# Kernel tuning notes

Measured on AMD Instinct MI355X. Metric: run time of the kernel, lower is better.

Reference implementation:

```python
import jax, jax.numpy as jnp
import numpy as np

N_NODES = 50000
N_REL = 4
N_EDGE = 160000
H = 128
OUT = 100
L_HID = 2
N_QUERY = 8192


def setup_inputs() -> dict:
    key = jax.random.key(0)
    ks = jax.random.split(key, 10)
    s = 1.0 / np.sqrt(H)
    return {
        "feature": jax.random.normal(ks[0], (N_NODES, H), dtype=jnp.float32),
        "Wr_h": jax.random.normal(ks[1], (L_HID, N_REL, H, H), dtype=jnp.float32) * s,
        "Ws_h": jax.random.normal(ks[2], (L_HID, H, H), dtype=jnp.float32) * s,
        "Wr_o": jax.random.normal(ks[3], (N_REL, H, OUT), dtype=jnp.float32) * s,
        "Ws_o": jax.random.normal(ks[4], (H, OUT), dtype=jnp.float32) * s,
        "edge_src": jax.random.randint(ks[5], (N_REL, N_EDGE), 0, N_NODES, dtype=jnp.int64),
        "edge_dst": jax.random.randint(ks[6], (N_REL, N_EDGE), 0, N_NODES, dtype=jnp.int64),
        "head_idx": jax.random.randint(ks[7], (N_QUERY,), 0, N_NODES, dtype=jnp.int64),
        "tail_idx": jax.random.randint(ks[8], (N_QUERY,), 0, N_NODES, dtype=jnp.int64),
    }


def _rgcn_layer(h, edge_src, edge_dst, inv_deg, Wr, Ws, activate):
    # per-relation gather of source features: [R, E, H]
    msgs = h[edge_src]
    # per-relation scatter-add into destination nodes: [R, N, H]
    agg = jax.vmap(lambda m, d: jax.ops.segment_sum(m, d, num_segments=h.shape[0]))(msgs, edge_dst)
    agg = agg * inv_deg[..., None]  # mean (right) normalization per relation
    out = h @ Ws + jnp.einsum("rnh,rho->no", agg, Wr)
    return jax.nn.relu(out) if activate else out


def reference(feature, Wr_h, Ws_h, Wr_o, Ws_o, edge_src, edge_dst, head_idx, tail_idx):
    n = feature.shape[0]
    # per-relation in-degree, computed once (graph structure is fixed)
    deg = jax.vmap(lambda d: jax.ops.segment_sum(
        jnp.ones(d.shape, feature.dtype), d, num_segments=n))(edge_dst)  # [R, N]
    inv_deg = 1.0 / jnp.maximum(deg, 1.0)
    h = feature
    for l in range(Wr_h.shape[0]):
        h = _rgcn_layer(h, edge_src, edge_dst, inv_deg, Wr_h[l], Ws_h[l], activate=True)
    h = _rgcn_layer(h, edge_src, edge_dst, inv_deg, Wr_o, Ws_o, activate=False)
    heads = h[head_idx]  # [Q, OUT]
    tails = h[tail_idx]  # [Q, OUT]
    return (heads, tails)
```

## Files before the change

### kernel.cpp

```cpp
#include <hip/hip_runtime.h>
#include <hip/hip_bf16.h>

#define NN 50000
#define NR 4
#define NE 160000
#define HD 128
#define OD 100
#define NQ 8192
#define NB_SCAN 196

#define NB_COUNT 2500
#define NB_CONV  6250
#define NB_PREPW 960

typedef __attribute__((ext_vector_type(8))) short bf16x8;
typedef __attribute__((ext_vector_type(4))) float f32x4;
typedef __attribute__((ext_vector_type(2))) float f32x2;
typedef __attribute__((ext_vector_type(4))) int int4v;

static __device__ __forceinline__ unsigned short f2bf(float f) {
    union { float f; unsigned int u; } v; v.f = f;
    unsigned int u = v.u;
    unsigned int r = u + 0x7FFFu + ((u >> 16) & 1u);
    return (unsigned short)(r >> 16);
}
static __device__ __forceinline__ float bflo(unsigned int v) {
    union { unsigned int u; float f; } x; x.u = v << 16; return x.f;
}
static __device__ __forceinline__ float bfhi(unsigned int v) {
    union { unsigned int u; float f; } x; x.u = v & 0xffff0000u; return x.f;
}


__global__ __launch_bounds__(256) void prep_merged_kernel(
        const int* __restrict__ edge_dst, int* __restrict__ deg,
        const float* __restrict__ feature, unsigned short* __restrict__ h,
        const float* __restrict__ Ws_h, const float* __restrict__ Wr_h,
        const float* __restrict__ Ws_o, const float* __restrict__ Wr_o,
        unsigned short* __restrict__ Wt) {
    const int b = blockIdx.x;
    if (b < NB_COUNT) {
        const int i = b * 256 + threadIdx.x;
        const int r = i / NE;
        atomicAdd(&deg[r * NN + edge_dst[i]], 1);
    } else if (b < NB_COUNT + NB_CONV) {
        const int i = ((b - NB_COUNT) * 256 + threadIdx.x) * 4;
        h[i + 0] = f2bf(feature[i + 0]);
        h[i + 1] = f2bf(feature[i + 1]);
        h[i + 2] = f2bf(feature[i + 2]);
        h[i + 3] = f2bf(feature[i + 3]);
    } else {
        const int idx = (b - NB_COUNT - NB_CONV) * 256 + threadIdx.x;
        const int l = idx / (128 * 640);
        const int rem = idx % (128 * 640);
        const int c = rem / 640;
        const int k = rem % 640;
        float v = 0.0f;
        if (l < 2) {
            if (k < HD) v = Ws_h[(l * HD + k) * HD + c];
            else {
                int r = (k - HD) >> 7, kk = (k - HD) & 127;
                v = Wr_h[((l * NR + r) * HD + kk) * HD + c];
            }
        } else if (c < OD) {
            if (k < HD) v = Ws_o[k * OD + c];
            else {
                int r = (k - HD) >> 7, kk = (k - HD) & 127;
                v = Wr_o[(r * HD + kk) * OD + c];
            }
        }
        Wt[idx] = f2bf(v);
    }
}


__global__ __launch_bounds__(256) void scanA_kernel(const int* __restrict__ deg,
                                                    int* __restrict__ excl,
                                                    int* __restrict__ bsum) {
    const int r = blockIdx.x / NB_SCAN;
    const int b = blockIdx.x % NB_SCAN;
    const int tid = threadIdx.x;
    const int idx = b * 256 + tid;
    int v = (idx < NN) ? deg[r * NN + idx] : 0;
    __shared__ int buf[256];
    buf[tid] = v; __syncthreads();
    int sum = v;
    for (int off = 1; off < 256; off <<= 1) {
        int t = (tid >= off) ? buf[tid - off] : 0;
        __syncthreads();
        sum += t; buf[tid] = sum;
        __syncthreads();
    }
    if (idx < NN) excl[r * NN + idx] = sum - v;
    if (tid == 255) bsum[r * NB_SCAN + b] = sum;
}

__global__ __launch_bounds__(256) void scanC_kernel(const int* __restrict__ excl,
                                                    const int* __restrict__ bsum,
                                                    int* __restrict__ row_start,
                                                    int* __restrict__ cursor) {
    const int r = blockIdx.x / NB_SCAN;
    const int b = blockIdx.x % NB_SCAN;
    const int tid = threadIdx.x;
    __shared__ int buf[256];
    buf[tid] = (tid < b) ? bsum[r * NB_SCAN + tid] : 0;
    __syncthreads();
    for (int off = 128; off > 0; off >>= 1) {
        if (tid < off) buf[tid] += buf[tid + off];
        __syncthreads();
    }
    const int prefix = buf[0];
    const int idx = b * 256 + tid;
    if (idx < NN) {
        int v = excl[r * NN + idx] + prefix;
        row_start[r * (NN + 1) + idx] = v;
        cursor[r * NN + idx] = v;
    }
    if (b == 0 && tid == 0) row_start[r * (NN + 1) + NN] = NE;
}

__global__ __launch_bounds__(256) void fill_csr_kernel(const int* __restrict__ edge_src,
                                                       const int* __restrict__ edge_dst,
                                                       int* __restrict__ cursor,
                                                       int* __restrict__ csr_src) {
    const int i = blockIdx.x * 256 + threadIdx.x;
    const int r = i / NE;
    const int dst = edge_dst[i];
    const int pos = atomicAdd(&cursor[r * NN + dst], 1);
    csr_src[r * NE + pos] = edge_src[i];
}


template<int MODE>
__global__ __launch_bounds__(512, 8)
void fused_kernel(const unsigned short* __restrict__ h,
                  const unsigned short* __restrict__ Bt,
                  const int* __restrict__ row_start,
                  const int* __restrict__ csr_src,
                  void* __restrict__ outp, int M) {
    __shared__ __align__(16) char lds[40960];
    const int tid = threadIdx.x;
    const int m0 = blockIdx.x * 32;
    const int lane = tid & 63;
    const int w = tid >> 6;

    {
        const int row = tid >> 4, kb = (tid & 15) * 16;
        int gr = m0 + row; if (gr >= M) gr = M - 1;
        int4v v = *(const int4v*)((const char*)h + (size_t)gr * 256 + kb);
        *(int4v*)(lds + row * 256 + (kb ^ ((row & 7) << 4))) = v;
    }

    {
        const int g = lane >> 4, li = lane & 15;
        const int* __restrict__ csr = csr_src + (size_t)g * NE;
        const char* hp = (const char*)h + li * 16;
        const int n0 = m0 + (w << 2);
        const int rsB = g * (NN + 1);

        int bnd[5];
#pragma unroll
        for (int i = 0; i < 5; i++) {
            int n = n0 + i; if (n > M) n = M;
            bnd[i] = row_start[rsB + n];
        }

#pragma unroll 1
        for (int i = 0; i < 4; ++i) {
            const int s = bnd[i], e = bnd[i + 1];

            int sj[8];
#pragma unroll
            for (int j = 0; j < 8; j++) sj[j] = (s + j < e) ? csr[s + j] : 0;

            int4v vj[8];
#pragma unroll
            for (int j = 0; j < 8; j++) {
                if (s + j < e) vj[j] = *(const int4v*)(hp + (size_t)sj[j] * 256);
                else           vj[j] = (int4v){0, 0, 0, 0};
            }
            __builtin_amdgcn_sched_barrier(0);

            f32x2 c0 = {0.f, 0.f}, c1 = {0.f, 0.f}, c2 = {0.f, 0.f}, c3 = {0.f, 0.f};
#pragma unroll
            for (int j = 0; j < 8; j++) {
                const unsigned int* vu = (const unsigned int*)&vj[j];
                c0 += (f32x2){bflo(vu[0]), bfhi(vu[0])};
                c1 += (f32x2){bflo(vu[1]), bfhi(vu[1])};
                c2 += (f32x2){bflo(vu[2]), bfhi(vu[2])};
                c3 += (f32x2){bflo(vu[3]), bfhi(vu[3])};
            }

            for (int t = s + 8; t < e; ++t) {
                const int src = csr[t];
                const int4v v = *(const int4v*)(hp + (size_t)src * 256);
                const unsigned int* vu = (const unsigned int*)&v;
                c0 += (f32x2){bflo(vu[0]), bfhi(vu[0])};
                c1 += (f32x2){bflo(vu[1]), bfhi(vu[1])};
                c2 += (f32x2){bflo(vu[2]), bfhi(vu[2])};
                c3 += (f32x2){bflo(vu[3]), bfhi(vu[3])};
            }

            const float inv = 1.0f / fmaxf((float)(e - s), 1.0f);
            unsigned int p0 = (unsigned int)f2bf(inv * c0[0]) | ((unsigned int)f2bf(inv * c0[1]) << 16);
            unsigned int p1 = (unsigned int)f2bf(inv * c1[0]) | ((unsigned int)f2bf(inv * c1[1]) << 16);
            unsigned int p2 = (unsigned int)f2bf(inv * c2[0]) | ((unsigned int)f2bf(inv * c2[1]) << 16);
            unsigned int p3 = (unsigned int)f2bf(inv * c3[0]) | ((unsigned int)f2bf(inv * c3[1]) << 16);
            const int row = (w << 2) + i;
            const int cb = g * 256 + li * 16;
            *(int4v*)(lds + 8192 + row * 1024 + (cb ^ ((row & 7) << 4))) =
                (int4v){(int)p0, (int)p1, (int)p2, (int)p3};
        }
    }

    const int lr = lane & 15;
    const int lg = lane >> 4;
    const char* bB = (const char*)Bt + (size_t)(w * 16 + lr) * 1280;
    bf16x8 bpre[4];
#pragma unroll
    for (int kb = 0; kb < 4; kb++)
        bpre[kb] = *(const bf16x8*)(bB + kb * 64 + lg * 16);

    __syncthreads();

    f32x4 acc[2];
    acc[0] = (f32x4){0.f, 0.f, 0.f, 0.f};
    acc[1] = (f32x4){0.f, 0.f, 0.f, 0.f};

    __builtin_amdgcn_s_setprio(1);
#pragma unroll
    for (int kb = 0; kb < 20; ++kb) {
        const int kByte = kb * 64 + lg * 16;
        bf16x8 bfr = (kb < 4) ? bpre[kb] : *(const bf16x8*)(bB + kByte);
#pragma unroll
        for (int mi = 0; mi < 2; mi++) {
            const int row = mi * 16 + lr;
            int off;
            if (kb < 4) off = row * 256 + (kByte ^ ((row & 7) << 4));
            else        off = 8192 + row * 1024 + ((kByte - 256) ^ ((row & 7) << 4));
            bf16x8 af = *(const bf16x8*)(lds + off);
            acc[mi] = __builtin_amdgcn_mfma_f32_16x16x32_bf16(af, bfr, acc[mi], 0, 0, 0);
        }
    }
    __builtin_amdgcn_s_setprio(0);

    __syncthreads();

    if (MODE == 0) {
#pragma unroll
        for (int mi = 0; mi < 2; mi++) {
            const int col = w * 16 + lr;
#pragma unroll
            for (int j = 0; j < 4; j++) {
                const int row = mi * 16 + lg * 4 + j;
                *(unsigned short*)(lds + row * 256 + ((col * 2) ^ ((row & 7) << 4))) =
                    f2bf(fmaxf(acc[mi][j], 0.f));
            }
        }
        __syncthreads();
        unsigned short* o = (unsigned short*)outp;
        const int row = tid >> 4, kb = (tid & 15) * 16;
        const int grow = m0 + row;
        if (grow < M)
            *(int4v*)((char*)o + (size_t)grow * 256 + kb) =
                *(const int4v*)(lds + row * 256 + (kb ^ ((row & 7) << 4)));
    } else {
#pragma unroll
        for (int mi = 0; mi < 2; mi++) {
            const int col = w * 16 + lr;
#pragma unroll
            for (int j = 0; j < 4; j++) {
                const int row = mi * 16 + lg * 4 + j;
                *(float*)(lds + row * 512 + ((col * 4) ^ ((row & 7) << 4))) = acc[mi][j];
            }
        }
        __syncthreads();
        float* o = (float*)outp;
#pragma unroll
        for (int i = 0; i < 2; i++) {
            const int c = tid + i * 512;
            const int row = c >> 5, o16 = (c & 31) * 16;
            const int grow = m0 + row;
            if (grow < M)
                *(int4v*)((char*)o + (size_t)grow * 512 + o16) =
                    *(const int4v*)(lds + row * 512 + (o16 ^ ((row & 7) << 4)));
        }
    }
}


__global__ __launch_bounds__(256) void gather_out_kernel(const float* __restrict__ hOut,
                                                         const int* __restrict__ head,
                                                         const int* __restrict__ tail,
                                                         float* __restrict__ out) {
    const int gid = blockIdx.x * 256 + threadIdx.x;
    const int q = gid >> 5, c = gid & 31;
    if (q >= 2 * NQ || c >= 25) return;
    const int node = (q < NQ) ? head[q] : tail[q - NQ];
    f32x4 v = *(const f32x4*)(hOut + (size_t)node * 128 + c * 4);
    *(f32x4*)(out + (size_t)q * OD + c * 4) = v;
}


extern "C" void kernel_launch(void* const* d_in, const int* in_sizes, int n_in,
                              void* d_out, int out_size, void* d_ws, size_t ws_size,
                              hipStream_t stream) {
    const float* feature = (const float*)d_in[0];
    const float* Wr_h    = (const float*)d_in[1];
    const float* Ws_h    = (const float*)d_in[2];
    const float* Wr_o    = (const float*)d_in[3];
    const float* Ws_o    = (const float*)d_in[4];
    const int* edge_src  = (const int*)d_in[5];
    const int* edge_dst  = (const int*)d_in[6];
    const int* head_idx  = (const int*)d_in[7];
    const int* tail_idx  = (const int*)d_in[8];
    float* out = (float*)d_out;

    char* ws = (char*)d_ws;
    size_t off = 0;
    auto alloc = [&](size_t bytes) -> void* {
        void* p = ws + off;
        off += (bytes + 255) & ~(size_t)255;
        return p;
    };
    unsigned short* hA   = (unsigned short*)alloc((size_t)NN * HD * 2);
    unsigned short* hB   = (unsigned short*)alloc((size_t)NN * HD * 2);
    float*          hOut = (float*)alloc((size_t)NN * 128 * 4);
    unsigned short* Wt   = (unsigned short*)alloc((size_t)3 * 128 * 640 * 2);
    int*            deg  = (int*)alloc((size_t)NR * NN * 4);
    int*            rowS = (int*)alloc((size_t)NR * (NN + 1) * 4);
    int*            curs = (int*)alloc((size_t)NR * NN * 4);
    int*            csrS = (int*)alloc((size_t)NR * NE * 4 + 64);
    int*            excl = (int*)alloc((size_t)NR * NN * 4);
    int*            bsum = (int*)alloc((size_t)NR * NB_SCAN * 4);
    (void)ws_size;

    hipMemsetAsync(deg, 0, (size_t)NR * NN * 4, stream);
    prep_merged_kernel<<<NB_COUNT + NB_CONV + NB_PREPW, 256, 0, stream>>>(
        edge_dst, deg, feature, hA, Ws_h, Wr_h, Ws_o, Wr_o, Wt);
    scanA_kernel<<<NR * NB_SCAN, 256, 0, stream>>>(deg, excl, bsum);
    scanC_kernel<<<NR * NB_SCAN, 256, 0, stream>>>(excl, bsum, rowS, curs);
    fill_csr_kernel<<<NB_COUNT, 256, 0, stream>>>(edge_src, edge_dst, curs, csrS);

    const int fblocks = (NN + 31) / 32;
    unsigned short* WtH0 = Wt;
    unsigned short* WtH1 = Wt + 128 * 640;
    unsigned short* WtO  = Wt + 2 * 128 * 640;

    fused_kernel<0><<<fblocks, 512, 0, stream>>>(hA, WtH0, rowS, csrS, hB, NN);
    fused_kernel<0><<<fblocks, 512, 0, stream>>>(hB, WtH1, rowS, csrS, hA, NN);
    fused_kernel<1><<<fblocks, 512, 0, stream>>>(hA, WtO,  rowS, csrS, hOut, NN);

    gather_out_kernel<<<(2 * NQ * 32 + 255) / 256, 256, 0, stream>>>(hOut, head_idx, tail_idx, out);
}
```

Baseline: 252.1 us.

## Replace CSR build with atomic ELL adjacency plus overflow list

```diff
diff --git a/kernel.cpp b/kernel.cpp
--- a/kernel.cpp
+++ b/kernel.cpp
@@ -7,9 +7,10 @@
 #define HD 128
 #define OD 100
 #define NQ 8192
-#define NB_SCAN 196
-
-#define NB_COUNT 2500
+#define ELL_CAP 16
+#define OVF_CAP 8192
+
+#define NB_BUILD 2500
 #define NB_CONV  6250
 #define NB_PREPW 960
 
@@ -33,24 +34,33 @@
 
 
 __global__ __launch_bounds__(256) void prep_merged_kernel(
-        const int* __restrict__ edge_dst, int* __restrict__ deg,
+        const int* __restrict__ edge_src, const int* __restrict__ edge_dst,
+        int* __restrict__ deg, int* __restrict__ ell,
+        int* __restrict__ ovf_cnt, int2* __restrict__ ovf,
         const float* __restrict__ feature, unsigned short* __restrict__ h,
         const float* __restrict__ Ws_h, const float* __restrict__ Wr_h,
         const float* __restrict__ Ws_o, const float* __restrict__ Wr_o,
         unsigned short* __restrict__ Wt) {
     const int b = blockIdx.x;
-    if (b < NB_COUNT) {
+    if (b < NB_BUILD) {
         const int i = b * 256 + threadIdx.x;
         const int r = i / NE;
-        atomicAdd(&deg[r * NN + edge_dst[i]], 1);
-    } else if (b < NB_COUNT + NB_CONV) {
-        const int i = ((b - NB_COUNT) * 256 + threadIdx.x) * 4;
+        const int key = (edge_dst[i] << 2) | r;
+        const int src = edge_src[i];
+        const int pos = atomicAdd(&deg[key], 1);
+        if (pos < ELL_CAP) ell[key * ELL_CAP + pos] = src;
+        else {
+            const int op = atomicAdd(ovf_cnt, 1);
+            if (op < OVF_CAP) ovf[op] = make_int2(key, src);
+        }
+    } else if (b < NB_BUILD + NB_CONV) {
+        const int i = ((b - NB_BUILD) * 256 + threadIdx.x) * 4;
         h[i + 0] = f2bf(feature[i + 0]);
         h[i + 1] = f2bf(feature[i + 1]);
         h[i + 2] = f2bf(feature[i + 2]);
         h[i + 3] = f2bf(feature[i + 3]);
     } else {
-        const int idx = (b - NB_COUNT - NB_CONV) * 256 + threadIdx.x;
+        const int idx = (b - NB_BUILD - NB_CONV) * 256 + threadIdx.x;
         const int l = idx / (128 * 640);
         const int rem = idx % (128 * 640);
         const int c = rem / 640;
@@ -74,69 +84,14 @@
 }
 
 
-__global__ __launch_bounds__(256) void scanA_kernel(const int* __restrict__ deg,
-                                                    int* __restrict__ excl,
-                                                    int* __restrict__ bsum) {
-    const int r = blockIdx.x / NB_SCAN;
-    const int b = blockIdx.x % NB_SCAN;
-    const int tid = threadIdx.x;
-    const int idx = b * 256 + tid;
-    int v = (idx < NN) ? deg[r * NN + idx] : 0;
-    __shared__ int buf[256];
-    buf[tid] = v; __syncthreads();
-    int sum = v;
-    for (int off = 1; off < 256; off <<= 1) {
-        int t = (tid >= off) ? buf[tid - off] : 0;
-        __syncthreads();
-        sum += t; buf[tid] = sum;
-        __syncthreads();
-    }
-    if (idx < NN) excl[r * NN + idx] = sum - v;
-    if (tid == 255) bsum[r * NB_SCAN + b] = sum;
-}
-
-__global__ __launch_bounds__(256) void scanC_kernel(const int* __restrict__ excl,
-                                                    const int* __restrict__ bsum,
-                                                    int* __restrict__ row_start,
-                                                    int* __restrict__ cursor) {
-    const int r = blockIdx.x / NB_SCAN;
-    const int b = blockIdx.x % NB_SCAN;
-    const int tid = threadIdx.x;
-    __shared__ int buf[256];
-    buf[tid] = (tid < b) ? bsum[r * NB_SCAN + tid] : 0;
-    __syncthreads();
-    for (int off = 128; off > 0; off >>= 1) {
-        if (tid < off) buf[tid] += buf[tid + off];
-        __syncthreads();
-    }
-    const int prefix = buf[0];
-    const int idx = b * 256 + tid;
-    if (idx < NN) {
-        int v = excl[r * NN + idx] + prefix;
-        row_start[r * (NN + 1) + idx] = v;
-        cursor[r * NN + idx] = v;
-    }
-    if (b == 0 && tid == 0) row_start[r * (NN + 1) + NN] = NE;
-}
-
-__global__ __launch_bounds__(256) void fill_csr_kernel(const int* __restrict__ edge_src,
-                                                       const int* __restrict__ edge_dst,
-                                                       int* __restrict__ cursor,
-                                                       int* __restrict__ csr_src) {
-    const int i = blockIdx.x * 256 + threadIdx.x;
-    const int r = i / NE;
-    const int dst = edge_dst[i];
-    const int pos = atomicAdd(&cursor[r * NN + dst], 1);
-    csr_src[r * NE + pos] = edge_src[i];
-}
-
-
 template<int MODE>
 __global__ __launch_bounds__(512, 8)
 void fused_kernel(const unsigned short* __restrict__ h,
                   const unsigned short* __restrict__ Bt,
-                  const int* __restrict__ row_start,
-                  const int* __restrict__ csr_src,
+                  const int* __restrict__ deg,
+                  const int* __restrict__ ell,
+                  const int* __restrict__ ovf_cnt,
+                  const int2* __restrict__ ovf,
                   void* __restrict__ outp, int M) {
     __shared__ __align__(16) char lds[40960];
     const int tid = threadIdx.x;
@@ -153,32 +108,29 @@
 
     {
         const int g = lane >> 4, li = lane & 15;
-        const int* __restrict__ csr = csr_src + (size_t)g * NE;
         const char* hp = (const char*)h + li * 16;
         const int n0 = m0 + (w << 2);
-        const int rsB = g * (NN + 1);
-
-        int bnd[5];
-#pragma unroll
-        for (int i = 0; i < 5; i++) {
-            int n = n0 + i; if (n > M) n = M;
-            bnd[i] = row_start[rsB + n];
-        }
 
 #pragma unroll 1
         for (int i = 0; i < 4; ++i) {
-            const int s = bnd[i], e = bnd[i + 1];
-
-            int sj[8];
-#pragma unroll
-            for (int j = 0; j < 8; j++) sj[j] = (s + j < e) ? csr[s + j] : 0;
+            const int n = n0 + i;
+            const int nc = (n < M) ? n : (M - 1);
+            const int key = (nc << 2) | g;
+            const int dg = (n < M) ? deg[key] : 0;
+            const int e = (dg < ELL_CAP) ? dg : ELL_CAP;
+            const int* eb = ell + ((size_t)key << 4);
+
+            const int4v s03 = *(const int4v*)(eb);
+            const int4v s47 = *(const int4v*)(eb + 4);
 
             int4v vj[8];
-#pragma unroll
-            for (int j = 0; j < 8; j++) {
-                if (s + j < e) vj[j] = *(const int4v*)(hp + (size_t)sj[j] * 256);
-                else           vj[j] = (int4v){0, 0, 0, 0};
-            }
+            const int4v z = {0, 0, 0, 0};
+#pragma unroll
+            for (int j = 0; j < 4; j++)
+                vj[j] = (j < e) ? *(const int4v*)(hp + (size_t)s03[j] * 256) : z;
+#pragma unroll
+            for (int j = 0; j < 4; j++)
+                vj[4 + j] = (4 + j < e) ? *(const int4v*)(hp + (size_t)s47[j] * 256) : z;
             __builtin_amdgcn_sched_barrier(0);
 
             f32x2 c0 = {0.f, 0.f}, c1 = {0.f, 0.f}, c2 = {0.f, 0.f}, c3 = {0.f, 0.f};
@@ -191,17 +143,43 @@
                 c3 += (f32x2){bflo(vu[3]), bfhi(vu[3])};
             }
 
-            for (int t = s + 8; t < e; ++t) {
-                const int src = csr[t];
-                const int4v v = *(const int4v*)(hp + (size_t)src * 256);
-                const unsigned int* vu = (const unsigned int*)&v;
-                c0 += (f32x2){bflo(vu[0]), bfhi(vu[0])};
-                c1 += (f32x2){bflo(vu[1]), bfhi(vu[1])};
-                c2 += (f32x2){bflo(vu[2]), bfhi(vu[2])};
-                c3 += (f32x2){bflo(vu[3]), bfhi(vu[3])};
-            }
-
-            const float inv = 1.0f / fmaxf((float)(e - s), 1.0f);
+            if (dg > 8) {
+                const int4v s8  = *(const int4v*)(eb + 8);
+                const int4v s12 = *(const int4v*)(eb + 12);
+                int4v wj[8];
+#pragma unroll
+                for (int j = 0; j < 4; j++)
+                    wj[j] = (8 + j < e) ? *(const int4v*)(hp + (size_t)s8[j] * 256) : z;
+#pragma unroll
+                for (int j = 0; j < 4; j++)
+                    wj[4 + j] = (12 + j < e) ? *(const int4v*)(hp + (size_t)s12[j] * 256) : z;
+#pragma unroll
+                for (int j = 0; j < 8; j++) {
+                    const unsigned int* vu = (const unsigned int*)&wj[j];
+                    c0 += (f32x2){bflo(vu[0]), bfhi(vu[0])};
+                    c1 += (f32x2){bflo(vu[1]), bfhi(vu[1])};
+                    c2 += (f32x2){bflo(vu[2]), bfhi(vu[2])};
+                    c3 += (f32x2){bflo(vu[3]), bfhi(vu[3])};
+                }
+            }
+
+            if (dg > ELL_CAP) {
+                int oc = ovf_cnt[0];
+                if (oc > OVF_CAP) oc = OVF_CAP;
+                for (int k = 0; k < oc; ++k) {
+                    const int2 ov = ovf[k];
+                    if (ov.x == key) {
+                        const int4v v = *(const int4v*)(hp + (size_t)ov.y * 256);
+                        const unsigned int* vu = (const unsigned int*)&v;
+                        c0 += (f32x2){bflo(vu[0]), bfhi(vu[0])};
+                        c1 += (f32x2){bflo(vu[1]), bfhi(vu[1])};
+                        c2 += (f32x2){bflo(vu[2]), bfhi(vu[2])};
+                        c3 += (f32x2){bflo(vu[3]), bfhi(vu[3])};
+                    }
+                }
+            }
+
+            const float inv = 1.0f / fmaxf((float)dg, 1.0f);
             unsigned int p0 = (unsigned int)f2bf(inv * c0[0]) | ((unsigned int)f2bf(inv * c0[1]) << 16);
             unsigned int p1 = (unsigned int)f2bf(inv * c1[0]) | ((unsigned int)f2bf(inv * c1[1]) << 16);
             unsigned int p2 = (unsigned int)f2bf(inv * c2[0]) | ((unsigned int)f2bf(inv * c2[1]) << 16);
@@ -328,28 +306,24 @@
     float*          hOut = (float*)alloc((size_t)NN * 128 * 4);
     unsigned short* Wt   = (unsigned short*)alloc((size_t)3 * 128 * 640 * 2);
     int*            deg  = (int*)alloc((size_t)NR * NN * 4);
-    int*            rowS = (int*)alloc((size_t)NR * (NN + 1) * 4);
-    int*            curs = (int*)alloc((size_t)NR * NN * 4);
-    int*            csrS = (int*)alloc((size_t)NR * NE * 4 + 64);
-    int*            excl = (int*)alloc((size_t)NR * NN * 4);
-    int*            bsum = (int*)alloc((size_t)NR * NB_SCAN * 4);
+    int*            ovfc = (int*)alloc(256);
+    int*            ell  = (int*)alloc((size_t)NR * NN * ELL_CAP * 4);
+    int2*           ovf  = (int2*)alloc((size_t)OVF_CAP * 8);
     (void)ws_size;
 
-    hipMemsetAsync(deg, 0, (size_t)NR * NN * 4, stream);
-    prep_merged_kernel<<<NB_COUNT + NB_CONV + NB_PREPW, 256, 0, stream>>>(
-        edge_dst, deg, feature, hA, Ws_h, Wr_h, Ws_o, Wr_o, Wt);
-    scanA_kernel<<<NR * NB_SCAN, 256, 0, stream>>>(deg, excl, bsum);
-    scanC_kernel<<<NR * NB_SCAN, 256, 0, stream>>>(excl, bsum, rowS, curs);
-    fill_csr_kernel<<<NB_COUNT, 256, 0, stream>>>(edge_src, edge_dst, curs, csrS);
+    hipMemsetAsync(deg, 0, (size_t)NR * NN * 4 + 256, stream);
+    prep_merged_kernel<<<NB_BUILD + NB_CONV + NB_PREPW, 256, 0, stream>>>(
+        edge_src, edge_dst, deg, ell, ovfc, ovf,
+        feature, hA, Ws_h, Wr_h, Ws_o, Wr_o, Wt);
 
     const int fblocks = (NN + 31) / 32;
     unsigned short* WtH0 = Wt;
     unsigned short* WtH1 = Wt + 128 * 640;
     unsigned short* WtO  = Wt + 2 * 128 * 640;
 
-    fused_kernel<0><<<fblocks, 512, 0, stream>>>(hA, WtH0, rowS, csrS, hB, NN);
-    fused_kernel<0><<<fblocks, 512, 0, stream>>>(hB, WtH1, rowS, csrS, hA, NN);
-    fused_kernel<1><<<fblocks, 512, 0, stream>>>(hA, WtO,  rowS, csrS, hOut, NN);
+    fused_kernel<0><<<fblocks, 512, 0, stream>>>(hA, WtH0, deg, ell, ovfc, ovf, hB, NN);
+    fused_kernel<0><<<fblocks, 512, 0, stream>>>(hB, WtH1, deg, ell, ovfc, ovf, hA, NN);
+    fused_kernel<1><<<fblocks, 512, 0, stream>>>(hA, WtO,  deg, ell, ovfc, ovf, hOut, NN);
 
     gather_out_kernel<<<(2 * NQ * 32 + 255) / 256, 256, 0, stream>>>(hOut, head_idx, tail_idx, out);
 }
```

Result: faster. 220.6 us (median of 2 runs) (-12.5%).
